# Kernel tuning notes

Hardware: AMD Instinct MI355X
Metric: run time of the kernel (lower is better)

The kernel has to match this reference:

```python
import jax, jax.numpy as jnp
import numpy as np

HEADS = 8
DIM_HEAD = 64
QUERY_DIM = 512
CONTEXT_DIM = 768
INNER_DIM = HEADS * DIM_HEAD  # 512
SCALE = DIM_HEAD ** -0.5


def setup_inputs() -> dict:
    key = jax.random.key(0)
    ks = jax.random.split(key, 7)
    B, N, M = 4, 2048, 1024
    x = jax.random.normal(ks[0], (B, N, QUERY_DIM), dtype=jnp.float32)
    context = jax.random.normal(ks[1], (B, M, CONTEXT_DIM), dtype=jnp.float32)
    # torch Linear weights stored as (out_features, in_features); y = x @ W.T
    Wq = jax.random.normal(ks[2], (INNER_DIM, QUERY_DIM), dtype=jnp.float32) * (QUERY_DIM ** -0.5)
    Wk = jax.random.normal(ks[3], (INNER_DIM, CONTEXT_DIM), dtype=jnp.float32) * (CONTEXT_DIM ** -0.5)
    Wv = jax.random.normal(ks[4], (INNER_DIM, CONTEXT_DIM), dtype=jnp.float32) * (CONTEXT_DIM ** -0.5)
    Wo = jax.random.normal(ks[5], (QUERY_DIM, INNER_DIM), dtype=jnp.float32) * (INNER_DIM ** -0.5)
    bo = jax.random.normal(ks[6], (QUERY_DIM,), dtype=jnp.float32) * 0.01
    return {"x": x, "context": context, "Wq": Wq, "Wk": Wk, "Wv": Wv, "Wo": Wo, "bo": bo}


def reference(x, context, Wq, Wk, Wv, Wo, bo):
    B, N, _ = x.shape
    M = context.shape[1]
    h, d = HEADS, DIM_HEAD
    q = jnp.einsum('bnc,ic->bni', x, Wq)        # [B,N,inner]
    k = jnp.einsum('bmc,ic->bmi', context, Wk)  # [B,M,inner]
    v = jnp.einsum('bmc,ic->bmi', context, Wv)  # [B,M,inner]
    # split heads: b n (h d) -> b h n d
    q = q.reshape(B, N, h, d).transpose(0, 2, 1, 3)
    k = k.reshape(B, M, h, d).transpose(0, 2, 1, 3)
    v = v.reshape(B, M, h, d).transpose(0, 2, 1, 3)
    # fp32 upcast for QK^T (inputs already fp32; kept explicit for fidelity)
    sim = jnp.einsum('bhnd,bhmd->bhnm', q.astype(jnp.float32), k.astype(jnp.float32)) * SCALE
    attn = jax.nn.softmax(sim, axis=-1)
    out = jnp.einsum('bhnm,bhmd->bhnd', attn, v)  # [B,h,N,d]
    out = out.transpose(0, 2, 1, 3).reshape(B, N, h * d)  # b n (h d)
    return jnp.einsum('bni,oi->bno', out, Wo) + bo  # dropout p=0 in eval
```

## Files before the change

### kernel.cpp

```cpp
#include <hip/hip_runtime.h>

using u16 = unsigned short;
typedef __bf16 bf16x8 __attribute__((ext_vector_type(8)));
typedef __bf16 bf16x2 __attribute__((ext_vector_type(2)));
typedef float  f32x4  __attribute__((ext_vector_type(4)));
typedef float  f32x16 __attribute__((ext_vector_type(16)));

#define MFMA16x16x32 __builtin_amdgcn_mfma_f32_16x16x32_bf16
#define MFMA32x32x16 __builtin_amdgcn_mfma_f32_32x32x16_bf16

#if __has_builtin(__builtin_amdgcn_exp2f)
#define EXP2 __builtin_amdgcn_exp2f
#else
#define EXP2 exp2f
#endif

static __device__ __forceinline__ unsigned f2bf_u(float f){
  unsigned x = __builtin_bit_cast(unsigned, f);
  return (x + 0x7fffu + ((x >> 16) & 1u)) >> 16;
}

static __device__ __forceinline__ void gll16(const void* g, void* l){
  __builtin_amdgcn_global_load_lds((const __attribute__((address_space(1))) void*)g,
                                   (__attribute__((address_space(3))) void*)l, 16, 0, 0);
}

static __device__ __forceinline__ f32x16 splat16(float x){
  f32x16 v;
#pragma unroll
  for (int i = 0; i < 16; ++i) v[i] = x;
  return v;
}

__global__ void __launch_bounds__(256) cvt_all(
    const float* __restrict__ x,  u16* __restrict__ xb,
    const float* __restrict__ cx, u16* __restrict__ cxb,
    const float* __restrict__ wq, u16* __restrict__ wqb,
    const float* __restrict__ wk, u16* __restrict__ wkb,
    const float* __restrict__ wv, u16* __restrict__ wvb,
    const float* __restrict__ wo, u16* __restrict__ wob)
{
  const float* in; u16* out; int n4;
  switch (blockIdx.y){
    case 0: in=x;  out=xb;  n4=(4*2048*512)/4; break;
    case 1: in=cx; out=cxb; n4=(4*1024*768)/4; break;
    case 2: in=wq; out=wqb; n4=(512*512)/4;    break;
    case 3: in=wk; out=wkb; n4=(512*768)/4;    break;
    case 4: in=wv; out=wvb; n4=(512*768)/4;    break;
    default:in=wo; out=wob; n4=(512*512)/4;    break;
  }
  int i = blockIdx.x*256 + threadIdx.x;
  const int stride = gridDim.x*256;
  for (; i < n4; i += stride){
    float4 f = ((const float4*)in)[i];
    ushort4 u;
    u.x = (u16)f2bf_u(f.x); u.y = (u16)f2bf_u(f.y);
    u.z = (u16)f2bf_u(f.z); u.w = (u16)f2bf_u(f.w);
    ((ushort4*)out)[i] = u;
  }
}

template<int LDA, int LDB, int KK, int OM>
static __device__ __forceinline__ void gemm_tile64(
    const u16* __restrict__ Ap, const u16* __restrict__ Bp,
    void* __restrict__ Cv, int ldc, int bx, int by,
    const float* __restrict__ bias, float scale,
    u16* __restrict__ sAp, u16* __restrict__ sBp)
{
  const int tid = threadIdx.x;
  const int w = tid >> 6, lane = tid & 63;
  const int wr = w >> 1, wc = w & 1;
  const long tm = (long)bx * 128;
  const long tn = (long)by * 64;

  f32x4 acc[4][2] = {};

  const int srl = lane >> 3, scc = lane & 7;

  auto stage = [&](int kt, int bb){
#pragma unroll
    for (int i = 0; i < 4; ++i){
      const int row = w*32 + i*8 + srl;
      const int sw = scc ^ (row & 7);
      gll16(Ap + (tm + row)*LDA + kt*64 + sw*8, sAp + bb*(128*64) + (w*32 + i*8)*64);
    }
#pragma unroll
    for (int i = 0; i < 2; ++i){
      const int row = w*16 + i*8 + srl;
      const int sw = scc ^ (row & 7);
      gll16(Bp + (tn + row)*LDB + kt*64 + sw*8, sBp + bb*(64*64) + (w*16 + i*8)*64);
    }
  };

  const int fr = lane & 15, fg = lane >> 4;
  constexpr int NK = KK / 64;

  stage(0, 0);
  __syncthreads();
  for (int kt = 0; kt < NK; ++kt){
    if (kt + 1 < NK) stage(kt + 1, (kt + 1) & 1);
    const int bb = kt & 1;
    bf16x8 af[4][2], bfr[2][2];
#pragma unroll
    for (int fm = 0; fm < 4; ++fm){
      const int row = wr*64 + fm*16 + fr;
      const int swz = row & 7;
#pragma unroll
      for (int s = 0; s < 2; ++s)
        af[fm][s] = *(const bf16x8*)&sAp[bb*(128*64) + row*64 + ((s*4 + fg) ^ swz)*8];
    }
#pragma unroll
    for (int fn = 0; fn < 2; ++fn){
      const int row = wc*32 + fn*16 + fr;
      const int swz = row & 7;
#pragma unroll
      for (int s = 0; s < 2; ++s)
        bfr[fn][s] = *(const bf16x8*)&sBp[bb*(64*64) + row*64 + ((s*4 + fg) ^ swz)*8];
    }
#pragma unroll
    for (int s = 0; s < 2; ++s)
#pragma unroll
      for (int fm = 0; fm < 4; ++fm)
#pragma unroll
        for (int fn = 0; fn < 2; ++fn)
          acc[fm][fn] = MFMA16x16x32(af[fm][s], bfr[fn][s], acc[fm][fn], 0, 0, 0);
    __syncthreads();
  }

#pragma unroll
  for (int fm = 0; fm < 4; ++fm){
#pragma unroll
    for (int fn = 0; fn < 2; ++fn){
      const long row0 = tm + wr*64 + fm*16 + fg*4;
      const long col  = tn + wc*32 + fn*16 + fr;
      if (OM == 0){
        u16* C = (u16*)Cv;
#pragma unroll
        for (int rr = 0; rr < 4; ++rr)
          C[(row0 + rr)*ldc + col] = (u16)f2bf_u(acc[fm][fn][rr] * scale);
      } else {
        float* C = (float*)Cv;
        const float bv = bias[col];
#pragma unroll
        for (int rr = 0; rr < 4; ++rr)
          C[(row0 + rr)*ldc + col] = acc[fm][fn][rr] + bv;
      }
    }
  }
}

template<int LDA, int LDB, int KK, int OM>
static __device__ __forceinline__ void gemm_tile128(
    const u16* __restrict__ Ap, const u16* __restrict__ Bp,
    void* __restrict__ Cv, int ldc, int bx, int by,
    const float* __restrict__ bias, float scale,
    u16* __restrict__ sAp, u16* __restrict__ sBp)
{
  const int tid = threadIdx.x;
  const int w = tid >> 6, lane = tid & 63;
  const int wr = w >> 1, wc = w & 1;
  const long tm = (long)bx * 128;
  const long tn = (long)by * 128;

  f32x4 acc[4][4] = {};

  const int srl = lane >> 3, scc = lane & 7;

  auto stage = [&](int kt, int bb){
#pragma unroll
    for (int i = 0; i < 4; ++i){
      const int row = w*32 + i*8 + srl;
      const int sw = scc ^ (row & 7);
      gll16(Ap + (tm + row)*LDA + kt*64 + sw*8, sAp + bb*(128*64) + (w*32 + i*8)*64);
      gll16(Bp + (tn + row)*LDB + kt*64 + sw*8, sBp + bb*(128*64) + (w*32 + i*8)*64);
    }
  };

  const int fr = lane & 15, fg = lane >> 4;
  constexpr int NK = KK / 64;

  stage(0, 0);
  __syncthreads();
  for (int kt = 0; kt < NK; ++kt){
    if (kt + 1 < NK) stage(kt + 1, (kt + 1) & 1);
    const int bb = kt & 1;
    bf16x8 af[4][2], bfr[4][2];
#pragma unroll
    for (int fm = 0; fm < 4; ++fm){
      const int row = wr*64 + fm*16 + fr;
      const int swz = row & 7;
#pragma unroll
      for (int s = 0; s < 2; ++s)
        af[fm][s] = *(const bf16x8*)&sAp[bb*(128*64) + row*64 + ((s*4 + fg) ^ swz)*8];
    }
#pragma unroll
    for (int fn = 0; fn < 4; ++fn){
      const int row = wc*64 + fn*16 + fr;
      const int swz = row & 7;
#pragma unroll
      for (int s = 0; s < 2; ++s)
        bfr[fn][s] = *(const bf16x8*)&sBp[bb*(128*64) + row*64 + ((s*4 + fg) ^ swz)*8];
    }
#pragma unroll
    for (int s = 0; s < 2; ++s)
#pragma unroll
      for (int fm = 0; fm < 4; ++fm)
#pragma unroll
        for (int fn = 0; fn < 4; ++fn)
          acc[fm][fn] = MFMA16x16x32(af[fm][s], bfr[fn][s], acc[fm][fn], 0, 0, 0);
    __syncthreads();
  }

#pragma unroll
  for (int fm = 0; fm < 4; ++fm){
#pragma unroll
    for (int fn = 0; fn < 4; ++fn){
      const long row0 = tm + wr*64 + fm*16 + fg*4;
      const long col  = tn + wc*64 + fn*16 + fr;
      if (OM == 0){
        u16* C = (u16*)Cv;
#pragma unroll
        for (int rr = 0; rr < 4; ++rr)
          C[(row0 + rr)*ldc + col] = (u16)f2bf_u(acc[fm][fn][rr] * scale);
      } else if (OM == 1){
        float* C = (float*)Cv;
        const float bv = bias[col];
#pragma unroll
        for (int rr = 0; rr < 4; ++rr)
          C[(row0 + rr)*ldc + col] = acc[fm][fn][rr] + bv;
      } else if (OM == 2){
        u16* C = (u16*)Cv;
        const int hh2 = (int)(col >> 6), d = (int)(col & 63);
        const int ks = d >> 4, hi2 = (d >> 3) & 1, e = d & 7;
#pragma unroll
        for (int rr = 0; rr < 4; ++rr){
          const long r = row0 + rr;
          const int b2 = (int)(r >> 10), m = (int)(r & 1023);
          const int tv = m >> 7, mtq = (m >> 5) & 3, q31r = m & 31;
          const long off = ((long)((((b2*8 + hh2)*8 + tv)*4 + mtq)*4 + ks))*512
                         + (hi2*32 + q31r)*8 + e;
          C[off] = (u16)f2bf_u(acc[fm][fn][rr] * scale);
        }
      } else {
        u16* C = (u16*)Cv;
        const int m = (int)col;
        const int tv = m >> 7, s = (m >> 4) & 7, hi2 = (m >> 3) & 1, e = m & 7;
#pragma unroll
        for (int rr = 0; rr < 4; ++rr){
          const int i = (int)(row0 + rr);
          const int hh2 = i >> 6, d0 = i & 63, fd = d0 >> 5, q31v = d0 & 31;
          const long off = ((long)((((hh2*8 + tv)*8 + s)*2 + fd)*2 + hi2))*256
                         + q31v*8 + e;
          C[off] = (u16)f2bf_u(acc[fm][fn][rr] * scale);
        }
      }
    }
  }
}

__global__ __launch_bounds__(256, 2) void proj_fused(
    const u16* __restrict__ xb,  const u16* __restrict__ cxb,
    const u16* __restrict__ wqb, const u16* __restrict__ wkb,
    const u16* __restrict__ wvb,
    u16* __restrict__ qb, u16* __restrict__ kpb, u16* __restrict__ vpb,
    float qscale)
{
  __shared__ u16 sA[2*128*64];
  __shared__ u16 sB[2*128*64];
  const int bid = blockIdx.x;
  const int lid = (bid & 7)*64 + (bid >> 3);
  if (lid < 256){
    gemm_tile128<512,512,512,0>(xb, wqb, (void*)qb, 512, lid >> 2, lid & 3,
                                nullptr, qscale, sA, sB);
  } else if (lid < 384){
    const int t = lid - 256;
    gemm_tile128<768,768,768,2>(cxb, wkb, (void*)kpb, 0, t >> 2, t & 3,
                                nullptr, 1.0f, sA, sB);
  } else {
    const int t = lid - 384, z = t >> 5, r = t & 31;
    gemm_tile128<768,768,768,3>(wvb, cxb + (long)z*1024*768,
                                (void*)(vpb + (long)z*524288), 0,
                                r >> 3, r & 7, nullptr, 1.0f, sA, sB);
  }
}

__global__ __launch_bounds__(256, 3) void gemm_out(
    const u16* __restrict__ ab, const u16* __restrict__ wob,
    float* __restrict__ out, const float* __restrict__ bias)
{
  __shared__ u16 sA[2*128*64];
  __shared__ u16 sB[2*64*64];
  const int bid = blockIdx.x;
  const int lid = (bid & 7)*64 + (bid >> 3);
  gemm_tile64<512,512,512,1>(ab, wob, (void*)out, 512, lid >> 3, lid & 7,
                             bias, 1.0f, sA, sB);
}

__global__ __launch_bounds__(512, 2) void attn_fwd(
    const u16* __restrict__ Q,
    const u16* __restrict__ Kp,
    const u16* __restrict__ Vp,
    u16* __restrict__ O)
{
  const int bid = blockIdx.x;
  const int lid = (bid & 7)*32 + (bid >> 3);
  const int qx = lid & 7, hh = (lid >> 3) & 7, b = lid >> 6;
  const int w = threadIdx.x >> 6, lane = threadIdx.x & 63;
  const int q31 = lane & 31, hi = lane >> 5;
  const int w4 = w & 3, kvg = w >> 2;
  const int q0 = qx*256 + w4*64;
  const int bh = b*8 + hh;

  __shared__ float sO[4*2*2*1280];
  __shared__ float sLsP[16*32];
  __shared__ float sLsT[8*32];

  const u16* Kb2 = Kp + (long)bh*65536 + lane*8;
  const u16* Vb2 = Vp + (long)bh*65536 + lane*8;

  bf16x8 qf[2][4];
#pragma unroll
  for (int j = 0; j < 2; ++j){
    const u16* qrow = Q + (long)(b*2048 + q0 + j*32 + q31)*512 + hh*64;
#pragma unroll
    for (int ks = 0; ks < 4; ++ks)
      qf[j][ks] = *(const bf16x8*)(qrow + ks*16 + hi*8);
  }

  f32x16 o[2][2] = {{splat16(0.f), splat16(0.f)}, {splat16(0.f), splat16(0.f)}};
  float lsum0 = 0.f, lsum1 = 0.f;

#pragma unroll 2
  for (int u = 0; u < 16; ++u){
    const int tv = kvg*4 + (u >> 2);
    const int mt = u & 3;
    const u16* kp = Kb2 + (long)((tv*4 + mt)*4)*512;
    bf16x8 kf0 = *(const bf16x8*)(kp);
    bf16x8 kf1 = *(const bf16x8*)(kp + 512);
    bf16x8 kf2 = *(const bf16x8*)(kp + 1024);
    bf16x8 kf3 = *(const bf16x8*)(kp + 1536);
    const u16* vp = Vb2 + (long)((tv*8 + mt*2)*2)*512;
    bf16x8 bv00 = *(const bf16x8*)(vp);
    bf16x8 bv01 = *(const bf16x8*)(vp + 512);
    bf16x8 bv10 = *(const bf16x8*)(vp + 1024);
    bf16x8 bv11 = *(const bf16x8*)(vp + 1536);

    f32x16 s0 = splat16(-16.f), s1 = splat16(-16.f);
    __builtin_amdgcn_s_setprio(1);
    s0 = MFMA32x32x16(kf0, qf[0][0], s0, 0, 0, 0);
    s1 = MFMA32x32x16(kf0, qf[1][0], s1, 0, 0, 0);
    s0 = MFMA32x32x16(kf1, qf[0][1], s0, 0, 0, 0);
    s1 = MFMA32x32x16(kf1, qf[1][1], s1, 0, 0, 0);
    s0 = MFMA32x32x16(kf2, qf[0][2], s0, 0, 0, 0);
    s1 = MFMA32x32x16(kf2, qf[1][2], s1, 0, 0, 0);
    s0 = MFMA32x32x16(kf3, qf[0][3], s0, 0, 0, 0);
    s1 = MFMA32x32x16(kf3, qf[1][3], s1, 0, 0, 0);
    __builtin_amdgcn_s_setprio(0);

#pragma unroll
    for (int r = 0; r < 16; ++r) s0[r] = EXP2(s0[r]);
#pragma unroll
    for (int r = 0; r < 16; ++r) s1[r] = EXP2(s1[r]);
    {
      float a0=s0[0]+s0[1], a1=s0[2]+s0[3], a2=s0[4]+s0[5], a3=s0[6]+s0[7];
      float a4=s0[8]+s0[9], a5=s0[10]+s0[11], a6=s0[12]+s0[13], a7=s0[14]+s0[15];
      lsum0 += ((a0+a1)+(a2+a3)) + ((a4+a5)+(a6+a7));
      float c0=s1[0]+s1[1], c1=s1[2]+s1[3], c2=s1[4]+s1[5], c3=s1[6]+s1[7];
      float c4=s1[8]+s1[9], c5=s1[10]+s1[11], c6=s1[12]+s1[13], c7=s1[14]+s1[15];
      lsum1 += ((c0+c1)+(c2+c3)) + ((c4+c5)+(c6+c7));
    }
    unsigned pk0[8], pk1[8];
#pragma unroll
    for (int p2 = 0; p2 < 8; ++p2){
      union { bf16x2 h; unsigned u; } t0, t1;
      t0.h[0] = (__bf16)s0[2*p2]; t0.h[1] = (__bf16)s0[2*p2 + 1]; pk0[p2] = t0.u;
      t1.h[0] = (__bf16)s1[2*p2]; t1.h[1] = (__bf16)s1[2*p2 + 1]; pk1[p2] = t1.u;
    }

#pragma unroll
    for (int sl2 = 0; sl2 < 2; ++sl2){
      union { unsigned u[4]; bf16x8 v; } pa0, pa1;
      {
        unsigned a = pk0[sl2*4 + 0], bq = pk0[sl2*4 + 2];
        asm volatile("v_permlane32_swap_b32 %0, %1" : "+v"(a), "+v"(bq));
        pa0.u[0] = a;  pa0.u[2] = bq;
        unsigned a2 = pk0[sl2*4 + 1], b2 = pk0[sl2*4 + 3];
        asm volatile("v_permlane32_swap_b32 %0, %1" : "+v"(a2), "+v"(b2));
        pa0.u[1] = a2; pa0.u[3] = b2;
      }
      {
        unsigned a = pk1[sl2*4 + 0], bq = pk1[sl2*4 + 2];
        asm volatile("v_permlane32_swap_b32 %0, %1" : "+v"(a), "+v"(bq));
        pa1.u[0] = a;  pa1.u[2] = bq;
        unsigned a2 = pk1[sl2*4 + 1], b2 = pk1[sl2*4 + 3];
        asm volatile("v_permlane32_swap_b32 %0, %1" : "+v"(a2), "+v"(b2));
        pa1.u[1] = a2; pa1.u[3] = b2;
      }
      const bf16x8 bvf0 = sl2 ? bv10 : bv00;
      const bf16x8 bvf1 = sl2 ? bv11 : bv01;
      __builtin_amdgcn_s_setprio(1);
      o[0][0] = MFMA32x32x16(pa0.v, bvf0, o[0][0], 0, 0, 0);
      o[1][0] = MFMA32x32x16(pa1.v, bvf0, o[1][0], 0, 0, 0);
      o[0][1] = MFMA32x32x16(pa0.v, bvf1, o[0][1], 0, 0, 0);
      o[1][1] = MFMA32x32x16(pa1.v, bvf1, o[1][1], 0, 0, 0);
      __builtin_amdgcn_s_setprio(0);
    }
  }

  lsum0 += __shfl_xor(lsum0, 32);
  lsum1 += __shfl_xor(lsum1, 32);
  sLsP[(w*2 + 0)*32 + q31] = lsum0;
  sLsP[(w*2 + 1)*32 + q31] = lsum1;
  __syncthreads();

  if (w >= 4){
#pragma unroll
    for (int j = 0; j < 2; ++j){
#pragma unroll
      for (int fd = 0; fd < 2; ++fd){
        float* p = sO + ((((w - 4)*2 + j)*2 + fd)*1280) + lane*20;
#pragma unroll
        for (int k = 0; k < 4; ++k){
          f32x4 t4;
#pragma unroll
          for (int e = 0; e < 4; ++e) t4[e] = o[j][fd][4*k + e];
          *(f32x4*)(p + 4*k) = t4;
        }
      }
    }
  }
  __syncthreads();

  if (w < 4){
#pragma unroll
    for (int j = 0; j < 2; ++j){
#pragma unroll
      for (int fd = 0; fd < 2; ++fd){
        const float* p = sO + (((w*2 + j)*2 + fd)*1280) + lane*20;
#pragma unroll
        for (int k = 0; k < 4; ++k){
          f32x4 t4 = *(const f32x4*)(p + 4*k);
#pragma unroll
          for (int e = 0; e < 4; ++e) o[j][fd][4*k + e] += t4[e];
        }
      }
    }
    const float lt0 = lsum0 + sLsP[((w + 4)*2 + 0)*32 + q31];
    const float lt1 = lsum1 + sLsP[((w + 4)*2 + 1)*32 + q31];
    sLsT[(w*2 + 0)*32 + q31] = lt0;
    sLsT[(w*2 + 1)*32 + q31] = lt1;
  }
  __syncthreads();

  if (w < 4){
#pragma unroll
    for (int j = 0; j < 2; ++j){
      f32x4 inv[4];
#pragma unroll
      for (int g = 0; g < 4; ++g){
        f32x4 ls = *(const f32x4*)&sLsT[(w*2 + j)*32 + 8*g + 4*hi];
#pragma unroll
        for (int e = 0; e < 4; ++e) inv[g][e] = 1.0f / ls[e];
      }
      u16* orow = O + (long)(b*2048 + q0 + j*32)*512 + hh*64;
#pragma unroll
      for (int fd = 0; fd < 2; ++fd){
#pragma unroll
        for (int r = 0; r < 16; ++r){
          const int q = (r & 3) + 8*(r >> 2) + 4*hi;
          const float val = o[j][fd][r] * inv[r >> 2][r & 3];
          orow[(long)q*512 + fd*32 + q31] = (u16)f2bf_u(val);
        }
      }
    }
  }
}

extern "C" void kernel_launch(void* const* d_in, const int* in_sizes, int n_in,
                              void* d_out, int out_size, void* d_ws, size_t ws_size,
                              hipStream_t stream)
{
  (void)in_sizes; (void)n_in; (void)out_size; (void)ws_size;
  const float* x   = (const float*)d_in[0];
  const float* ctx = (const float*)d_in[1];
  const float* Wq  = (const float*)d_in[2];
  const float* Wk  = (const float*)d_in[3];
  const float* Wv  = (const float*)d_in[4];
  const float* Wo  = (const float*)d_in[5];
  const float* bo  = (const float*)d_in[6];
  float* out = (float*)d_out;

  char* ws = (char*)d_ws;
  u16* xb  = (u16*)(ws + 0);
  u16* cxb = (u16*)(ws + 8388608);
  u16* wqb = (u16*)(ws + 14680064);
  u16* wkb = (u16*)(ws + 15204352);
  u16* wvb = (u16*)(ws + 15990784);
  u16* wob = (u16*)(ws + 16777216);
  u16* qb  = (u16*)(ws + 17301504);
  u16* kpb = (u16*)(ws + 25690112);
  u16* vpb = (u16*)(ws + 29884416);
  u16* ab  = (u16*)(ws + 34078720);

  cvt_all<<<dim3(1024, 6, 1), 256, 0, stream>>>(x, xb, ctx, cxb, Wq, wqb,
                                                Wk, wkb, Wv, wvb, Wo, wob);

  proj_fused<<<dim3(512, 1, 1), 256, 0, stream>>>(
      xb, cxb, wqb, wkb, wvb, qb, kpb, vpb, 0.18033688011112042f);

  attn_fwd<<<dim3(256, 1, 1), 512, 0, stream>>>(qb, kpb, vpb, ab);

  gemm_out<<<dim3(512, 1, 1), 256, 0, stream>>>(ab, wob, out, bo);
}
```

Baseline: 68.60 us.

## Split attention KV range across four wave groups and double grid size

Each attention block now covers 128 queries instead of 256, and the four waves sharing a query slice each take a quarter of the KV range instead of half. The grid grows from 256 to 512 blocks to fill more CUs on the device. In exchange, the partial output accumulators are reduced in a two-step tree through shared memory with extra barriers, and each block does more reduction work relative to its compute.

```diff
diff --git a/kernel.cpp b/kernel.cpp
--- a/kernel.cpp
+++ b/kernel.cpp
@@ -303,17 +303,17 @@
     u16* __restrict__ O)
 {
   const int bid = blockIdx.x;
-  const int lid = (bid & 7)*32 + (bid >> 3);
-  const int qx = lid & 7, hh = (lid >> 3) & 7, b = lid >> 6;
+  const int lid = (bid & 7)*64 + (bid >> 3);
+  const int qx = lid & 15, hh = (lid >> 4) & 7, b = lid >> 7;
   const int w = threadIdx.x >> 6, lane = threadIdx.x & 63;
   const int q31 = lane & 31, hi = lane >> 5;
-  const int w4 = w & 3, kvg = w >> 2;
-  const int q0 = qx*256 + w4*64;
+  const int qw = w >> 2, g = w & 3;
+  const int q0 = qx*128 + qw*64;
   const int bh = b*8 + hh;
 
-  __shared__ float sO[4*2*2*1280];
+  __shared__ float sO[16384];
   __shared__ float sLsP[16*32];
-  __shared__ float sLsT[8*32];
+  __shared__ float sLsT[4*32];
 
   const u16* Kb2 = Kp + (long)bh*65536 + lane*8;
   const u16* Vb2 = Vp + (long)bh*65536 + lane*8;
@@ -331,8 +331,8 @@
   float lsum0 = 0.f, lsum1 = 0.f;
 
 #pragma unroll 2
-  for (int u = 0; u < 16; ++u){
-    const int tv = kvg*4 + (u >> 2);
+  for (int u = 0; u < 8; ++u){
+    const int tv = g*2 + (u >> 2);
     const int mt = u & 3;
     const u16* kp = Kb2 + (long)((tv*4 + mt)*4)*512;
     bf16x8 kf0 = *(const bf16x8*)(kp);
@@ -413,54 +413,90 @@
   sLsP[(w*2 + 1)*32 + q31] = lsum1;
   __syncthreads();
 
-  if (w >= 4){
+  {
+    const int base = (((qw*2 + 0)*2 + 0)*64 + lane)*16;
+    if (g == 1 || g == 3){
+      float* R = sO + (g == 3 ? 8192 : 0);
+#pragma unroll
+      for (int j = 0; j < 2; ++j)
+#pragma unroll
+        for (int fd = 0; fd < 2; ++fd){
+          float* p = R + base + (j*2 + fd)*64*16;
+#pragma unroll
+          for (int k = 0; k < 4; ++k){
+            f32x4 t4;
+#pragma unroll
+            for (int e = 0; e < 4; ++e) t4[e] = o[j][fd][4*k + e];
+            *(f32x4*)(p + 4*k) = t4;
+          }
+        }
+    }
+    __syncthreads();
+    if (g == 0 || g == 2){
+      const float* R = sO + (g == 2 ? 8192 : 0);
+#pragma unroll
+      for (int j = 0; j < 2; ++j)
+#pragma unroll
+        for (int fd = 0; fd < 2; ++fd){
+          const float* p = R + base + (j*2 + fd)*64*16;
+#pragma unroll
+          for (int k = 0; k < 4; ++k){
+            f32x4 t4 = *(const f32x4*)(p + 4*k);
+#pragma unroll
+            for (int e = 0; e < 4; ++e) o[j][fd][4*k + e] += t4[e];
+          }
+        }
+    }
+    __syncthreads();
+    if (g == 2){
+#pragma unroll
+      for (int j = 0; j < 2; ++j)
+#pragma unroll
+        for (int fd = 0; fd < 2; ++fd){
+          float* p = sO + base + (j*2 + fd)*64*16;
+#pragma unroll
+          for (int k = 0; k < 4; ++k){
+            f32x4 t4;
+#pragma unroll
+            for (int e = 0; e < 4; ++e) t4[e] = o[j][fd][4*k + e];
+            *(f32x4*)(p + 4*k) = t4;
+          }
+        }
+    }
+    __syncthreads();
+    if (g == 0){
+#pragma unroll
+      for (int j = 0; j < 2; ++j)
+#pragma unroll
+        for (int fd = 0; fd < 2; ++fd){
+          const float* p = sO + base + (j*2 + fd)*64*16;
+#pragma unroll
+          for (int k = 0; k < 4; ++k){
+            f32x4 t4 = *(const f32x4*)(p + 4*k);
+#pragma unroll
+            for (int e = 0; e < 4; ++e) o[j][fd][4*k + e] += t4[e];
+          }
+        }
+    }
+  }
+
+  if (g == 0){
 #pragma unroll
     for (int j = 0; j < 2; ++j){
-#pragma unroll
-      for (int fd = 0; fd < 2; ++fd){
-        float* p = sO + ((((w - 4)*2 + j)*2 + fd)*1280) + lane*20;
-#pragma unroll
-        for (int k = 0; k < 4; ++k){
-          f32x4 t4;
-#pragma unroll
-          for (int e = 0; e < 4; ++e) t4[e] = o[j][fd][4*k + e];
-          *(f32x4*)(p + 4*k) = t4;
-        }
-      }
-    }
-  }
-  __syncthreads();
-
-  if (w < 4){
-#pragma unroll
-    for (int j = 0; j < 2; ++j){
-#pragma unroll
-      for (int fd = 0; fd < 2; ++fd){
-        const float* p = sO + (((w*2 + j)*2 + fd)*1280) + lane*20;
-#pragma unroll
-        for (int k = 0; k < 4; ++k){
-          f32x4 t4 = *(const f32x4*)(p + 4*k);
-#pragma unroll
-          for (int e = 0; e < 4; ++e) o[j][fd][4*k + e] += t4[e];
-        }
-      }
-    }
-    const float lt0 = lsum0 + sLsP[((w + 4)*2 + 0)*32 + q31];
-    const float lt1 = lsum1 + sLsP[((w + 4)*2 + 1)*32 + q31];
-    sLsT[(w*2 + 0)*32 + q31] = lt0;
-    sLsT[(w*2 + 1)*32 + q31] = lt1;
-  }
-  __syncthreads();
-
-  if (w < 4){
+      float lt = 0.f;
+#pragma unroll
+      for (int gg = 0; gg < 4; ++gg)
+        lt += sLsP[((qw*4 + gg)*2 + j)*32 + q31];
+      sLsT[(qw*2 + j)*32 + q31] = lt;
+    }
 #pragma unroll
     for (int j = 0; j < 2; ++j){
       f32x4 inv[4];
 #pragma unroll
-      for (int g = 0; g < 4; ++g){
-        f32x4 ls = *(const f32x4*)&sLsT[(w*2 + j)*32 + 8*g + 4*hi];
-#pragma unroll
-        for (int e = 0; e < 4; ++e) inv[g][e] = 1.0f / ls[e];
+      for (int gq = 0; gq < 4; ++gq){
+        f32x4 ls = *(const f32x4*)&sLsT[(qw*2 + j)*32 + 8*gq + 4*hi];
+#pragma unroll
+        for (int e = 0; e < 4; ++e) inv[gq][e] = 1.0f / ls[e];
       }
       u16* orow = O + (long)(b*2048 + q0 + j*32)*512 + hh*64;
 #pragma unroll
@@ -508,7 +544,7 @@
   proj_fused<<<dim3(512, 1, 1), 256, 0, stream>>>(
       xb, cxb, wqb, wkb, wvb, qb, kpb, vpb, 0.18033688011112042f);
 
-  attn_fwd<<<dim3(256, 1, 1), 512, 0, stream>>>(qb, kpb, vpb, ab);
+  attn_fwd<<<dim3(512, 1, 1), 512, 0, stream>>>(qb, kpb, vpb, ab);
 
   gemm_out<<<dim3(512, 1, 1), 256, 0, stream>>>(ab, wob, out, bo);
 }
```

Measured after the change: 77.39 us. 1.13x slower.
